# Kernel tuning notes

Hardware: AMD Instinct MI355X
Metric: run time of the kernel (lower is better)

Reference implementation:

```python
import jax, jax.numpy as jnp
import numpy as np

N = 4096
IN_F = 256
OUT_F = 32
H = 8
NEG_SLOPE = 0.2
EDGE_P = 0.004  # avg degree ~16


def setup_inputs() -> dict:
    key = jax.random.key(0)
    k1, k2, k3, k4, k5 = jax.random.split(key, 5)
    x = jax.random.normal(k1, (N, IN_F), dtype=jnp.float32)
    adj = jax.random.bernoulli(k2, EDGE_P, (N, N))  # bool sparse-ish adjacency
    # xavier-uniform-ish scales
    w_scale = np.sqrt(6.0 / (IN_F + OUT_F))
    a_scale = np.sqrt(6.0 / (OUT_F + 1))
    W = jax.random.uniform(k3, (H, IN_F, OUT_F), jnp.float32, -w_scale, w_scale)
    a_src = jax.random.uniform(k4, (H, OUT_F), jnp.float32, -a_scale, a_scale)
    a_dst = jax.random.uniform(k5, (H, OUT_F), jnp.float32, -a_scale, a_scale)
    bias = jnp.zeros((H * OUT_F,), dtype=jnp.float32)
    return {"x": x, "adj": adj, "W": W, "a_src": a_src, "a_dst": a_dst, "bias": bias}


def reference(x, adj, W, a_src, a_dst, bias):
    n = x.shape[0]
    # adjacency mask with self-loops, (N, N)
    mask = adj | jnp.eye(n, dtype=bool)
    # Wh: (H, N, OUT_F)
    Wh = jnp.einsum('hif,ni->hnf', W, x)
    # per-node attention logits, (H, N)
    e_src = jnp.einsum('hnf,hf->hn', Wh, a_src)
    e_dst = jnp.einsum('hnf,hf->hn', Wh, a_dst)
    # additive scores, (H, N, N): row i attends over columns j
    e = e_src[:, :, None] + e_dst[:, None, :]
    e = jnp.where(e >= 0, e, NEG_SLOPE * e)  # LeakyReLU
    e = jnp.where(mask[None], e, -jnp.inf)
    alpha = jax.nn.softmax(e, axis=-1)
    # dropout p=0.6 is a no-op in eval mode
    out = jnp.einsum('hnm,hmf->hnf', alpha, Wh)
    # concat heads: (N, H*OUT_F)
    out = jnp.transpose(out, (1, 0, 2)).reshape(n, -1)
    return out + bias
```

## Files before the change

kernel.cpp:

```cpp
#include <hip/hip_runtime.h>
#include <hip/hip_bf16.h>
#include <stdint.h>

#define N_NODES 4096
#define IN_F 256
#define OUT_F 32
#define H 8
#define HF 256
#define NPB 8
#define MAXK 128

typedef __hip_bfloat16 bf16;
__device__ __forceinline__ float b2f(bf16 v) { return __bfloat162float(v); }

__global__ __launch_bounds__(256) void detect_kernel(
    const uint16_t* __restrict__ x, const uint32_t* __restrict__ adj,
    int* __restrict__ modes)
{
    __shared__ int s[4];
    const int t = threadIdx.x;
    if (t < 4) s[t] = 0;
    __syncthreads();
    int wild = 0, E = 0, F = 0, G = 0;
    for (int i = t; i < 2048; i += 256) {
        uint16_t u = x[i];
        bf16 v = *(bf16*)&u;
        float f = b2f(v);
        if (!(fabsf(f) < 100.0f)) wild++;
    }
    for (int i = t; i < 16384; i += 256) {
        uint32_t w = adj[i];
        if ((w >> 8) != 0) E++;
        uint32_t lo = w & 0xFFFFu, hi = w >> 16;
        if (lo == 0x3F80u || hi == 0x3F80u) F++;
        if (lo != 0) G++;
    }
    if (wild) atomicAdd(&s[0], wild);
    if (E)    atomicAdd(&s[1], E);
    if (F)    atomicAdd(&s[2], F);
    if (G)    atomicAdd(&s[3], G);
    __syncthreads();
    if (t == 0) {
        int f32m = s[0] > 32;
        int amode;
        if (s[1] == 0)                 amode = 0;
        else if (s[2] > 0 && s[3]==0)  amode = 0;
        else if (s[2] > 0)             amode = 1;
        else                           amode = 2;
        modes[0] = f32m | (amode << 1);
    }
}

__global__ __launch_bounds__(256) void wh_kernel(
    const void* __restrict__ xv, const void* __restrict__ Wv,
    const void* __restrict__ asv, const void* __restrict__ adv,
    const int* __restrict__ modes,
    float* __restrict__ Wh, float* __restrict__ esrc, float* __restrict__ edst)
{
    __shared__ float xl[NPB][IN_F];
    const int t = threadIdx.x;
    const int n0 = blockIdx.x * NPB;
    const int f32m = modes[0] & 1;

    if (f32m) {
        const float* x = (const float*)xv;
        #pragma unroll
        for (int r = 0; r < NPB; ++r) xl[r][t] = x[(size_t)(n0 + r) * IN_F + t];
    } else {
        const bf16* x = (const bf16*)xv;
        #pragma unroll
        for (int r = 0; r < NPB; ++r) xl[r][t] = b2f(x[(size_t)(n0 + r) * IN_F + t]);
    }
    __syncthreads();

    const int h = t >> 5, f = t & 31;
    float acc[NPB];
    #pragma unroll
    for (int r = 0; r < NPB; ++r) acc[r] = 0.f;

    if (f32m) {
        const float* Wp = (const float*)Wv + (size_t)h * IN_F * OUT_F + f;
        #pragma unroll 8
        for (int i = 0; i < IN_F; ++i) {
            float w = Wp[i * OUT_F];
            #pragma unroll
            for (int r = 0; r < NPB; ++r) acc[r] += xl[r][i] * w;
        }
    } else {
        const bf16* Wp = (const bf16*)Wv + (size_t)h * IN_F * OUT_F + f;
        #pragma unroll 8
        for (int i = 0; i < IN_F; ++i) {
            float w = b2f(Wp[i * OUT_F]);
            #pragma unroll
            for (int r = 0; r < NPB; ++r) acc[r] += xl[r][i] * w;
        }
    }

    float as, ad;
    if (f32m) { as = ((const float*)asv)[t]; ad = ((const float*)adv)[t]; }
    else      { as = b2f(((const bf16*)asv)[t]); ad = b2f(((const bf16*)adv)[t]); }

    #pragma unroll
    for (int r = 0; r < NPB; ++r) {
        Wh[(size_t)(n0 + r) * HF + t] = acc[r];
        float vs = acc[r] * as, vd = acc[r] * ad;
        for (int off = 16; off > 0; off >>= 1) {
            vs += __shfl_down(vs, off, 32);
            vd += __shfl_down(vd, off, 32);
        }
        if (f == 0) {
            esrc[(size_t)(n0 + r) * H + h] = vs;
            edst[(size_t)(n0 + r) * H + h] = vd;
        }
    }
}

__global__ __launch_bounds__(256) void gat_kernel(
    const void* __restrict__ adjv, const float* __restrict__ Wh,
    const float* __restrict__ esrc, const float* __restrict__ edst,
    const void* __restrict__ biasv, const int* __restrict__ modes,
    void* __restrict__ outv)
{
    __shared__ int   nbr[MAXK];
    __shared__ float sc[MAXK * H];
    __shared__ float inv_s[H];
    __shared__ int   cnt;

    const int i = blockIdx.x, t = threadIdx.x;
    if (t == 0) cnt = 0;
    __syncthreads();

    const int m = modes[0];
    const int amode = m >> 1;
    auto push = [&](int j) { int p = atomicAdd(&cnt, 1); if (p < MAXK) nbr[p] = j; };

    if (amode == 0) {
        const int4* row = (const int4*)((const uint32_t*)adjv + (size_t)i * N_NODES);
        for (int c = t; c < N_NODES / 4; c += 256) {
            int4 v = row[c]; int j0 = c * 4;
            if (v.x != 0 && j0     != i) push(j0);
            if (v.y != 0 && j0 + 1 != i) push(j0 + 1);
            if (v.z != 0 && j0 + 2 != i) push(j0 + 2);
            if (v.w != 0 && j0 + 3 != i) push(j0 + 3);
        }
    } else if (amode == 1) {
        const int4* row = (const int4*)((const uint16_t*)adjv + (size_t)i * N_NODES);
        for (int c = t; c < N_NODES / 8; c += 256) {
            int4 v = row[c]; int j0 = c * 8;
            uint32_t w[4] = {(uint32_t)v.x, (uint32_t)v.y, (uint32_t)v.z, (uint32_t)v.w};
            #pragma unroll
            for (int q = 0; q < 4; ++q) {
                int b0 = j0 + 2 * q;
                if ((w[q] & 0xFFFFu) && b0     != i) push(b0);
                if ((w[q] >> 16)     && b0 + 1 != i) push(b0 + 1);
            }
        }
    } else {
        const int4* row = (const int4*)((const uint8_t*)adjv + (size_t)i * N_NODES);
        for (int c = t; c < N_NODES / 16; c += 256) {
            int4 v = row[c]; int j0 = c * 16;
            uint32_t w[4] = {(uint32_t)v.x, (uint32_t)v.y, (uint32_t)v.z, (uint32_t)v.w};
            #pragma unroll
            for (int q = 0; q < 4; ++q) {
                uint32_t u = w[q]; int b0 = j0 + 4 * q;
                if ((u & 0x000000FFu) && b0     != i) push(b0);
                if ((u & 0x0000FF00u) && b0 + 1 != i) push(b0 + 1);
                if ((u & 0x00FF0000u) && b0 + 2 != i) push(b0 + 2);
                if ((u & 0xFF000000u) && b0 + 3 != i) push(b0 + 3);
            }
        }
    }
    if (t == 0) push(i);
    __syncthreads();
    const int K = cnt < MAXK ? cnt : MAXK;

    const float* esrc_i = esrc + (size_t)i * H;
    for (int idx = t; idx < K * H; idx += 256) {
        int k = idx >> 3, h = idx & 7;
        float s = esrc_i[h] + edst[(size_t)nbr[k] * H + h];
        sc[idx] = s >= 0.f ? s : 0.2f * s;
    }
    __syncthreads();

    if (t < H) {
        float mx = -1e30f;
        for (int k = 0; k < K; ++k) mx = fmaxf(mx, sc[k * H + t]);
        float sum = 0.f;
        for (int k = 0; k < K; ++k) {
            float e = __expf(sc[k * H + t] - mx);
            sc[k * H + t] = e;
            sum += e;
        }
        inv_s[t] = 1.f / sum;
    }
    __syncthreads();

    const int h = t >> 5;
    float acc = 0.f;
    #pragma unroll 4
    for (int k = 0; k < K; ++k)
        acc += sc[k * H + h] * Wh[(size_t)nbr[k] * HF + t];

    const int f32m = m & 1;
    float bias = f32m ? ((const float*)biasv)[t] : b2f(((const bf16*)biasv)[t]);
    float o = acc * inv_s[h] + bias;
    if (f32m) ((float*)outv)[(size_t)i * HF + t] = o;
    else      ((bf16*)outv)[(size_t)i * HF + t] = __float2bfloat16(o);
}

extern "C" void kernel_launch(void* const* d_in, const int* in_sizes, int n_in,
                              void* d_out, int out_size, void* d_ws, size_t ws_size,
                              hipStream_t stream) {
    const void* x     = d_in[0];
    const void* adj   = d_in[1];
    const void* W     = d_in[2];
    const void* a_src = d_in[3];
    const void* a_dst = d_in[4];
    const void* bias  = d_in[5];

    int*   modes = (int*)d_ws;
    float* Wh    = (float*)((char*)d_ws + 256);
    float* esrc  = Wh + (size_t)N_NODES * HF;
    float* edst  = esrc + (size_t)N_NODES * H;

    detect_kernel<<<1, 256, 0, stream>>>((const uint16_t*)x, (const uint32_t*)adj, modes);
    wh_kernel<<<N_NODES / NPB, 256, 0, stream>>>(x, W, a_src, a_dst, modes, Wh, esrc, edst);
    gat_kernel<<<N_NODES, 256, 0, stream>>>(adj, Wh, esrc, edst, bias, modes, d_out);
}
```

Before: 147.0 us.

## Register-tile the Wh projection and fold dtype detection into it

Removes the separate single-block detect kernel. Each wh block now detects the float dtype by itself with a wavefront ballot over 64 x values, and an extra block computes the adjacency mode. The projection now computes a 4x4 register tile per thread over 16 nodes per block, using float4 weight loads and a transposed, padded shared x tile, so each weight and x value is reused more often. This saves one kernel launch and raises arithmetic intensity. The trade-off is that the dtype check now looks at a smaller sample of x.

```diff
diff --git a/kernel.cpp b/kernel.cpp
--- a/kernel.cpp
+++ b/kernel.cpp
@@ -7,110 +7,144 @@
 #define OUT_F 32
 #define H 8
 #define HF 256
-#define NPB 8
+#define NPB 16
+#define XPAD 20
 #define MAXK 128
 
 typedef __hip_bfloat16 bf16;
 __device__ __forceinline__ float b2f(bf16 v) { return __bfloat162float(v); }
 
-__global__ __launch_bounds__(256) void detect_kernel(
-    const uint16_t* __restrict__ x, const uint32_t* __restrict__ adj,
-    int* __restrict__ modes)
-{
-    __shared__ int s[4];
-    const int t = threadIdx.x;
-    if (t < 4) s[t] = 0;
-    __syncthreads();
-    int wild = 0, E = 0, F = 0, G = 0;
-    for (int i = t; i < 2048; i += 256) {
-        uint16_t u = x[i];
-        bf16 v = *(bf16*)&u;
-        float f = b2f(v);
-        if (!(fabsf(f) < 100.0f)) wild++;
-    }
-    for (int i = t; i < 16384; i += 256) {
-        uint32_t w = adj[i];
-        if ((w >> 8) != 0) E++;
-        uint32_t lo = w & 0xFFFFu, hi = w >> 16;
-        if (lo == 0x3F80u || hi == 0x3F80u) F++;
-        if (lo != 0) G++;
-    }
-    if (wild) atomicAdd(&s[0], wild);
-    if (E)    atomicAdd(&s[1], E);
-    if (F)    atomicAdd(&s[2], F);
-    if (G)    atomicAdd(&s[3], G);
-    __syncthreads();
-    if (t == 0) {
-        int f32m = s[0] > 32;
-        int amode;
-        if (s[1] == 0)                 amode = 0;
-        else if (s[2] > 0 && s[3]==0)  amode = 0;
-        else if (s[2] > 0)             amode = 1;
-        else                           amode = 2;
-        modes[0] = f32m | (amode << 1);
-    }
+__device__ __forceinline__ int detect_f32m(const void* xv, int t) {
+    uint16_t u = ((const uint16_t*)xv)[t & 63];
+    bf16 v = *(bf16*)&u;
+    float f = b2f(v);
+    int wild = !(fabsf(f) < 100.0f);
+    unsigned long long ball = __ballot(wild);
+    return __popcll(ball) > 4;
 }
 
 __global__ __launch_bounds__(256) void wh_kernel(
     const void* __restrict__ xv, const void* __restrict__ Wv,
     const void* __restrict__ asv, const void* __restrict__ adv,
-    const int* __restrict__ modes,
+    const uint32_t* __restrict__ adj, int* __restrict__ modes,
     float* __restrict__ Wh, float* __restrict__ esrc, float* __restrict__ edst)
 {
-    __shared__ float xl[NPB][IN_F];
     const int t = threadIdx.x;
+    const int f32m = detect_f32m(xv, t);
+
+    if (blockIdx.x == 256) {
+        __shared__ int s[4];
+        if (t < 4) s[t] = 0;
+        __syncthreads();
+        int E = 0, F = 0, G = 0;
+        for (int i = t; i < 16384; i += 256) {
+            uint32_t w = adj[i];
+            if ((w >> 8) != 0) E++;
+            uint32_t lo = w & 0xFFFFu, hi = w >> 16;
+            if (lo == 0x3F80u || hi == 0x3F80u) F++;
+            if (lo != 0) G++;
+        }
+        if (E) atomicAdd(&s[1], E);
+        if (F) atomicAdd(&s[2], F);
+        if (G) atomicAdd(&s[3], G);
+        __syncthreads();
+        if (t == 0) {
+            int amode;
+            if (s[1] == 0)               amode = 0;
+            else if (s[2] > 0 && !s[3])  amode = 0;
+            else if (s[2] > 0)           amode = 1;
+            else                         amode = 2;
+            modes[0] = f32m | (amode << 1);
+        }
+        return;
+    }
+
+    __shared__ float xl[IN_F][XPAD];
     const int n0 = blockIdx.x * NPB;
-    const int f32m = modes[0] & 1;
 
     if (f32m) {
-        const float* x = (const float*)xv;
+        const float* x = (const float*)xv + (size_t)n0 * IN_F;
         #pragma unroll
-        for (int r = 0; r < NPB; ++r) xl[r][t] = x[(size_t)(n0 + r) * IN_F + t];
-    } else {
-        const bf16* x = (const bf16*)xv;
+        for (int r = 0; r < NPB; ++r) xl[t][r] = x[(size_t)r * IN_F + t];
+    } else {
+        const bf16* x = (const bf16*)xv + (size_t)n0 * IN_F;
         #pragma unroll
-        for (int r = 0; r < NPB; ++r) xl[r][t] = b2f(x[(size_t)(n0 + r) * IN_F + t]);
-    }
-    __syncthreads();
-
-    const int h = t >> 5, f = t & 31;
-    float acc[NPB];
+        for (int r = 0; r < NPB; ++r) xl[t][r] = b2f(x[(size_t)r * IN_F + t]);
+    }
+    __syncthreads();
+
+    const int rg = t >> 6;
+    const int cg = t & 63;
+    const int h  = cg >> 3;
+    const int f0 = (cg & 7) * 4;
+
+    float acc[4][4];
     #pragma unroll
-    for (int r = 0; r < NPB; ++r) acc[r] = 0.f;
+    for (int r = 0; r < 4; ++r)
+        #pragma unroll
+        for (int j = 0; j < 4; ++j) acc[r][j] = 0.f;
 
     if (f32m) {
-        const float* Wp = (const float*)Wv + (size_t)h * IN_F * OUT_F + f;
-        #pragma unroll 8
+        const float* Wp = (const float*)Wv + (size_t)h * IN_F * OUT_F + f0;
+        #pragma unroll 4
         for (int i = 0; i < IN_F; ++i) {
-            float w = Wp[i * OUT_F];
-            #pragma unroll
-            for (int r = 0; r < NPB; ++r) acc[r] += xl[r][i] * w;
-        }
-    } else {
-        const bf16* Wp = (const bf16*)Wv + (size_t)h * IN_F * OUT_F + f;
-        #pragma unroll 8
+            const float4 w4 = *(const float4*)&Wp[(size_t)i * OUT_F];
+            const float4 x4 = *(const float4*)&xl[i][rg * 4];
+            const float xs[4] = {x4.x, x4.y, x4.z, x4.w};
+            #pragma unroll
+            for (int r = 0; r < 4; ++r) {
+                acc[r][0] += xs[r] * w4.x;
+                acc[r][1] += xs[r] * w4.y;
+                acc[r][2] += xs[r] * w4.z;
+                acc[r][3] += xs[r] * w4.w;
+            }
+        }
+    } else {
+        const bf16* Wp = (const bf16*)Wv + (size_t)h * IN_F * OUT_F + f0;
+        #pragma unroll 4
         for (int i = 0; i < IN_F; ++i) {
-            float w = b2f(Wp[i * OUT_F]);
-            #pragma unroll
-            for (int r = 0; r < NPB; ++r) acc[r] += xl[r][i] * w;
-        }
-    }
-
-    float as, ad;
-    if (f32m) { as = ((const float*)asv)[t]; ad = ((const float*)adv)[t]; }
-    else      { as = b2f(((const bf16*)asv)[t]); ad = b2f(((const bf16*)adv)[t]); }
+            const ushort4 wu = *(const ushort4*)&Wp[(size_t)i * OUT_F];
+            float w0 = b2f(*(bf16*)&wu.x), w1 = b2f(*(bf16*)&wu.y);
+            float w2 = b2f(*(bf16*)&wu.z), w3 = b2f(*(bf16*)&wu.w);
+            const float4 x4 = *(const float4*)&xl[i][rg * 4];
+            const float xs[4] = {x4.x, x4.y, x4.z, x4.w};
+            #pragma unroll
+            for (int r = 0; r < 4; ++r) {
+                acc[r][0] += xs[r] * w0;
+                acc[r][1] += xs[r] * w1;
+                acc[r][2] += xs[r] * w2;
+                acc[r][3] += xs[r] * w3;
+            }
+        }
+    }
+
+    float as0, as1, as2, as3, ad0, ad1, ad2, ad3;
+    if (f32m) {
+        const float4 a4 = *(const float4*)&((const float*)asv)[h * OUT_F + f0];
+        const float4 b4 = *(const float4*)&((const float*)adv)[h * OUT_F + f0];
+        as0 = a4.x; as1 = a4.y; as2 = a4.z; as3 = a4.w;
+        ad0 = b4.x; ad1 = b4.y; ad2 = b4.z; ad3 = b4.w;
+    } else {
+        const ushort4 a4 = *(const ushort4*)&((const bf16*)asv)[h * OUT_F + f0];
+        const ushort4 b4 = *(const ushort4*)&((const bf16*)adv)[h * OUT_F + f0];
+        as0 = b2f(*(bf16*)&a4.x); as1 = b2f(*(bf16*)&a4.y);
+        as2 = b2f(*(bf16*)&a4.z); as3 = b2f(*(bf16*)&a4.w);
+        ad0 = b2f(*(bf16*)&b4.x); ad1 = b2f(*(bf16*)&b4.y);
+        ad2 = b2f(*(bf16*)&b4.z); ad3 = b2f(*(bf16*)&b4.w);
+    }
 
     #pragma unroll
-    for (int r = 0; r < NPB; ++r) {
-        Wh[(size_t)(n0 + r) * HF + t] = acc[r];
-        float vs = acc[r] * as, vd = acc[r] * ad;
-        for (int off = 16; off > 0; off >>= 1) {
-            vs += __shfl_down(vs, off, 32);
-            vd += __shfl_down(vd, off, 32);
-        }
-        if (f == 0) {
-            esrc[(size_t)(n0 + r) * H + h] = vs;
-            edst[(size_t)(n0 + r) * H + h] = vd;
+    for (int r = 0; r < 4; ++r) {
+        const int n = n0 + rg * 4 + r;
+        *(float4*)&Wh[(size_t)n * HF + cg * 4] =
+            make_float4(acc[r][0], acc[r][1], acc[r][2], acc[r][3]);
+        float vs = acc[r][0] * as0 + acc[r][1] * as1 + acc[r][2] * as2 + acc[r][3] * as3;
+        float vd = acc[r][0] * ad0 + acc[r][1] * ad1 + acc[r][2] * ad2 + acc[r][3] * ad3;
+        vs += __shfl_down(vs, 4, 8); vs += __shfl_down(vs, 2, 8); vs += __shfl_down(vs, 1, 8);
+        vd += __shfl_down(vd, 4, 8); vd += __shfl_down(vd, 2, 8); vd += __shfl_down(vd, 1, 8);
+        if ((cg & 7) == 0) {
+            esrc[(size_t)n * H + h] = vs;
+            edst[(size_t)n * H + h] = vd;
         }
     }
 }
@@ -223,7 +257,7 @@
     float* esrc  = Wh + (size_t)N_NODES * HF;
     float* edst  = esrc + (size_t)N_NODES * H;
 
-    detect_kernel<<<1, 256, 0, stream>>>((const uint16_t*)x, (const uint32_t*)adj, modes);
-    wh_kernel<<<N_NODES / NPB, 256, 0, stream>>>(x, W, a_src, a_dst, modes, Wh, esrc, edst);
+    wh_kernel<<<N_NODES / NPB + 1, 256, 0, stream>>>(
+        x, W, a_src, a_dst, (const uint32_t*)adj, modes, Wh, esrc, edst);
     gat_kernel<<<N_NODES, 256, 0, stream>>>(adj, Wh, esrc, edst, bias, modes, d_out);
 }
```

After: 137.6 us. 6.4% less time.
